# Kernel optimization log

Hardware: AMD Instinct MI355X
Metric: run time of the kernel (lower is better)

Reference implementation:

```python
import jax, jax.numpy as jnp
import numpy as np

MEM_SLOTS = 8
HEAD = 64
HEADS = 16
MEM = HEAD * HEADS          # 1024
QKV = 3 * HEAD * HEADS      # 3072
B = 4096


def _layernorm(x, g, b, eps=1e-5):
    m = jnp.mean(x, axis=-1, keepdims=True)
    v = jnp.var(x, axis=-1, keepdims=True)
    return (x - m) * jax.lax.rsqrt(v + eps) * g + b


def setup_inputs() -> dict:
    key = jax.random.key(0)
    ks = jax.random.split(key, 16)
    def gw(k, shape, scale=0.02):
        return jax.random.normal(k, shape, jnp.float32) * scale
    return {
        "input_vec": jax.random.normal(ks[0], (B, MEM), jnp.float32),
        "memory": jax.random.normal(ks[1], (B, MEM_SLOTS, MEM), jnp.float32),
        # weights stored [in, out] (transpose of torch Linear.weight; same math)
        "qkv_w": gw(ks[2], (MEM, QKV)), "qkv_b": jnp.zeros((QKV,), jnp.float32),
        "qkvn_g": jnp.ones((QKV,), jnp.float32), "qkvn_b": jnp.zeros((QKV,), jnp.float32),
        "mlp1_w": gw(ks[3], (MEM, MEM)), "mlp1_b": jnp.zeros((MEM,), jnp.float32),
        "mlp2_w": gw(ks[4], (MEM, MEM)), "mlp2_b": jnp.zeros((MEM,), jnp.float32),
        "n1_g": jnp.ones((MEM,), jnp.float32), "n1_b": jnp.zeros((MEM,), jnp.float32),
        "n2_g": jnp.ones((MEM,), jnp.float32), "n2_b": jnp.zeros((MEM,), jnp.float32),
        "inp_w": gw(ks[5], (MEM, MEM)), "inp_b": jnp.zeros((MEM,), jnp.float32),
        "ig_w": gw(ks[6], (MEM, 2 * MEM)), "ig_b": jnp.zeros((2 * MEM,), jnp.float32),
        "mg_w": gw(ks[7], (MEM, 2 * MEM)), "mg_b": jnp.zeros((2 * MEM,), jnp.float32),
        "forget_bias": jnp.asarray(1.0, jnp.float32),
        "input_bias": jnp.asarray(0.0, jnp.float32),
    }


def reference(input_vec, memory, qkv_w, qkv_b, qkvn_g, qkvn_b,
              mlp1_w, mlp1_b, mlp2_w, mlp2_b, n1_g, n1_b, n2_g, n2_b,
              inp_w, inp_b, ig_w, ig_b, mg_w, mg_b, forget_bias, input_bias):
    # project input and append as extra slot: [B, N=mem_slots+1, MEM]
    inp = (input_vec @ inp_w + inp_b)[:, None, :]
    m = jnp.concatenate([memory, inp], axis=1)
    Bsz, N, _ = m.shape

    # fused qkv + layernorm, split into heads: [B, N, H, 3, hd]
    qkv = _layernorm(m @ qkv_w + qkv_b, qkvn_g, qkvn_b).reshape(Bsz, N, HEADS, 3, HEAD)
    q, k, v = qkv[..., 0, :], qkv[..., 1, :], qkv[..., 2, :]
    scale = HEAD ** -0.5
    attn = jax.nn.softmax(jnp.einsum('bnhd,bmhd->bhnm', q * scale, k), axis=-1)
    attended = jnp.einsum('bhnm,bmhd->bnhd', attn, v).reshape(Bsz, N, MEM)

    m = _layernorm(m + attended, n1_g, n1_b)
    mlp = jax.nn.relu(m @ mlp1_w + mlp1_b) @ mlp2_w + mlp2_b
    m = _layernorm(m + mlp, n2_g, n2_b)

    next_memory = m[:, :-1, :]  # drop input slot

    # LSTM-style gating ('unit' style)
    gates = (memory @ mg_w + mg_b) + (inp @ ig_w + ig_b)  # [B, mem_slots, 2*MEM]
    i_gate, f_gate = jnp.split(gates, 2, axis=-1)
    i_gate = jax.nn.sigmoid(i_gate + input_bias)
    f_gate = jax.nn.sigmoid(f_gate + forget_bias)
    next_memory = i_gate * jnp.tanh(next_memory) + f_gate * memory

    output = next_memory.reshape(Bsz, -1)
    return output, next_memory
```

## Files before the change

### kernel.cpp

```cpp
#include <hip/hip_runtime.h>
#include <stdint.h>

typedef __attribute__((ext_vector_type(8))) short s16x8;
typedef __attribute__((ext_vector_type(4))) float f32x4;

__device__ __forceinline__ float bf2f(unsigned short u) {
  union { unsigned int i; float f; } x; x.i = ((unsigned int)u) << 16; return x.f;
}
__device__ __forceinline__ unsigned short f2bf(float f) {
  union { float f; unsigned int i; } x; x.f = f;
  return (unsigned short)((x.i + 0x7FFFu + ((x.i >> 16) & 1u)) >> 16);
}
__device__ __forceinline__ void gload16(const unsigned short* g, unsigned short* l) {
  __builtin_amdgcn_global_load_lds((const __attribute__((address_space(1))) void*)g,
                                   (__attribute__((address_space(3))) void*)l, 16, 0, 0);
}

__global__ void wtrans_kernel(const float* __restrict__ w, unsigned short* __restrict__ wt,
                              int K, int N) {
  __shared__ float tile[32][33];
  const int n0 = blockIdx.x * 32, k0 = blockIdx.y * 32;
  const int tx = threadIdx.x, ty = threadIdx.y;
  for (int r = 0; r < 32; r += 8)
    tile[ty + r][tx] = w[(size_t)(k0 + ty + r) * N + n0 + tx];
  __syncthreads();
  for (int r = 0; r < 32; r += 8)
    wt[(size_t)(n0 + ty + r) * K + k0 + tx] = f2bf(tile[tx][ty + r]);
}

__global__ void cvt_f32_bf16(const float* __restrict__ src, unsigned short* __restrict__ dst, int n4) {
  int i = blockIdx.x * blockDim.x + threadIdx.x;
  const int stride = gridDim.x * blockDim.x;
  for (; i < n4; i += stride) {
    float4 v = ((const float4*)src)[i];
    ushort4 o; o.x = f2bf(v.x); o.y = f2bf(v.y); o.z = f2bf(v.z); o.w = f2bf(v.w);
    ((ushort4*)dst)[i] = o;
  }
}

template<int AMODE, int EPI>
__global__ void __launch_bounds__(256)
gemm_bt(const unsigned short* __restrict__ A,
        const unsigned short* __restrict__ A2,
        const unsigned short* __restrict__ Bt,
        const float* __restrict__ bias,
        const unsigned short* __restrict__ igp,
        const float* __restrict__ sib,
        const float* __restrict__ sfb,
        unsigned short* __restrict__ C,
        int tilesN, int N, int K)
{
  __shared__ __align__(16) unsigned short As[128 * 32];
  __shared__ __align__(16) unsigned short Bs[128 * 32];
  const int t = threadIdx.x;
  const int w = t >> 6, l = t & 63;

  const int nwg = gridDim.x;
  const int cpx = nwg >> 3;
  const int lid = blockIdx.x;
  const int wgid = (lid & 7) * cpx + (lid >> 3);
  const int bty = wgid / tilesN;
  const int btx = wgid - bty * tilesN;
  const int brow = bty << 7, bcol = btx << 7;
  const int wr = w >> 1, wc = w & 1;

  const unsigned short* ap[2];
  const unsigned short* bp[2];
  unsigned short* al[2];
  unsigned short* bl[2];
#pragma unroll
  for (int p0 = 0; p0 < 2; ++p0) {
    const int byteoff = ((p0 * 4 + w) << 10) + (l << 4);
    const int row = byteoff >> 6;
    const int ce  = (byteoff & 63) >> 1;
    const int ar  = brow + row;
    if (AMODE == 0) {
      ap[p0] = A + (size_t)ar * K + ce;
    } else {
      const int bb = ar / 9;
      const int nn = ar - bb * 9;
      ap[p0] = (nn < 8 ? (A + ((size_t)(bb * 8 + nn)) * K) : (A2 + (size_t)bb * K)) + ce;
    }
    bp[p0] = Bt + (size_t)(bcol + row) * K + ce;
    al[p0] = As + ((p0 * 4 + w) << 9);
    bl[p0] = Bs + ((p0 * 4 + w) << 9);
  }

  f32x4 acc[4][4] = {};
  const int kiters = K >> 5;
  for (int kt = 0; kt < kiters; ++kt) {
#pragma unroll
    for (int p0 = 0; p0 < 2; ++p0) {
      gload16(ap[p0], al[p0]);
      gload16(bp[p0], bl[p0]);
      ap[p0] += 32; bp[p0] += 32;
    }
    __syncthreads();
    const int lr = l & 15, lk = (l >> 4) << 3;
    s16x8 af[4], bfr[4];
#pragma unroll
    for (int m = 0; m < 4; ++m)
      af[m] = *(const s16x8*)(As + ((wr * 64 + m * 16 + lr) << 5) + lk);
#pragma unroll
    for (int n = 0; n < 4; ++n)
      bfr[n] = *(const s16x8*)(Bs + ((wc * 64 + n * 16 + lr) << 5) + lk);
#pragma unroll
    for (int m = 0; m < 4; ++m)
#pragma unroll
      for (int n = 0; n < 4; ++n)
        acc[m][n] = __builtin_amdgcn_mfma_f32_16x16x32_bf16(af[m], bfr[n], acc[m][n], 0, 0, 0);
    __syncthreads();
  }

  float ib = 0.f, fb = 0.f;
  if constexpr (EPI == 3) { ib = sib[0]; fb = sfb[0]; }
  const int row0 = brow + wr * 64 + ((l >> 4) << 2);
  const int col0 = bcol + wc * 64 + (l & 15);
#pragma unroll
  for (int m = 0; m < 4; ++m) {
#pragma unroll
    for (int n = 0; n < 4; ++n) {
      const int col = col0 + n * 16;
      const float bv = bias[col];
#pragma unroll
      for (int j = 0; j < 4; ++j) {
        const int row = row0 + m * 16 + j;
        float x = acc[m][n][j] + bv;
        if constexpr (EPI == 1) x = fmaxf(x, 0.f);
        if constexpr (EPI == 3) {
          x += bf2f(igp[(size_t)(row >> 3) * 2048 + col]);
          x += (col < 1024) ? ib : fb;
          x = 1.f / (1.f + expf(-x));
        }
        C[(size_t)row * N + col] = f2bf(x);
      }
    }
  }
}

#define QROW 3080
__global__ void __launch_bounds__(256)
attn_fused(const unsigned short* __restrict__ qkv,
           const float* __restrict__ g3, const float* __restrict__ b3,
           const float* __restrict__ memF,
           const float* __restrict__ g1, const float* __restrict__ b1,
           unsigned short* __restrict__ m1)
{
  __shared__ __align__(16) unsigned short sQ[9 * QROW];
  __shared__ float sS[16][8][12];
  __shared__ __align__(16) unsigned short sAtt[8 * 1024];
  const int b = blockIdx.x;
  const int t = threadIdx.x;
  const int wv = t >> 6, l = t & 63;

  const unsigned short* src = qkv + (size_t)b * (9 * 3072);
  for (int i = t; i < 3456; i += 256) {
    const int r = i / 384;
    const int c = i - r * 384;
    ((uint4*)(sQ + r * QROW))[c] = ((const uint4*)src)[i];
  }
  __syncthreads();

  for (int r = wv; r < 9; r += 4) {
    float s = 0.f, s2 = 0.f;
    for (int i = l; i < 3072; i += 64) {
      const float x = bf2f(sQ[r * QROW + i]); s += x; s2 += x * x;
    }
#pragma unroll
    for (int o = 32; o; o >>= 1) { s += __shfl_xor(s, o); s2 += __shfl_xor(s2, o); }
    const float mean = s * (1.f / 3072.f);
    const float rstd = rsqrtf(s2 * (1.f / 3072.f) - mean * mean + 1e-5f);
    for (int i = l; i < 3072; i += 64) {
      const float x = bf2f(sQ[r * QROW + i]);
      sQ[r * QROW + i] = f2bf((x - mean) * rstd * g3[i] + b3[i]);
    }
  }
  __syncthreads();

  for (int idx = t; idx < 1152; idx += 256) {
    const int h = idx / 72;
    const int rem = idx - h * 72;
    const int n = rem / 9;
    const int m = rem - n * 9;
    const ushort4* q4 = (const ushort4*)(sQ + n * QROW + h * 192);
    const ushort4* k4 = (const ushort4*)(sQ + m * QROW + h * 192 + 64);
    float acc = 0.f;
#pragma unroll
    for (int d = 0; d < 16; ++d) {
      const ushort4 qa = q4[d], ka = k4[d];
      acc += bf2f(qa.x) * bf2f(ka.x) + bf2f(qa.y) * bf2f(ka.y)
           + bf2f(qa.z) * bf2f(ka.z) + bf2f(qa.w) * bf2f(ka.w);
    }
    sS[h][n][m] = acc * 0.125f;
  }
  __syncthreads();

  if (t < 128) {
    const int h = t >> 3, n = t & 7;
    float mx = -1e30f;
#pragma unroll
    for (int m = 0; m < 9; ++m) mx = fmaxf(mx, sS[h][n][m]);
    float p[9]; float sum = 0.f;
#pragma unroll
    for (int m = 0; m < 9; ++m) { p[m] = expf(sS[h][n][m] - mx); sum += p[m]; }
    const float inv = 1.f / sum;
#pragma unroll
    for (int m = 0; m < 9; ++m) sS[h][n][m] = p[m] * inv;
  }
  __syncthreads();

  for (int o4 = t; o4 < 2048; o4 += 256) {
    const int n = o4 >> 8;
    const int rem = o4 & 255;
    const int h = rem >> 4;
    const int d4 = rem & 15;
    float a0 = 0, a1 = 0, a2 = 0, a3 = 0;
#pragma unroll
    for (int m = 0; m < 9; ++m) {
      const float pm = sS[h][n][m];
      const ushort4 vv = *(const ushort4*)(sQ + m * QROW + h * 192 + 128 + d4 * 4);
      a0 += pm * bf2f(vv.x); a1 += pm * bf2f(vv.y); a2 += pm * bf2f(vv.z); a3 += pm * bf2f(vv.w);
    }
    ushort4 ov; ov.x = f2bf(a0); ov.y = f2bf(a1); ov.z = f2bf(a2); ov.w = f2bf(a3);
    ((ushort4*)sAtt)[o4] = ov;
  }
  __syncthreads();

  const float* memb = memF + (size_t)b * 8192;
  for (int n = wv; n < 8; n += 4) {
    float xs[16]; float s = 0.f, s2 = 0.f;
#pragma unroll
    for (int j = 0; j < 16; ++j) {
      const int i = j * 64 + l;
      const float x = memb[n * 1024 + i] + bf2f(sAtt[n * 1024 + i]);
      xs[j] = x; s += x; s2 += x * x;
    }
#pragma unroll
    for (int o = 32; o; o >>= 1) { s += __shfl_xor(s, o); s2 += __shfl_xor(s2, o); }
    const float mean = s * (1.f / 1024.f);
    const float rstd = rsqrtf(s2 * (1.f / 1024.f) - mean * mean + 1e-5f);
    unsigned short* dst = m1 + ((size_t)b * 8 + n) * 1024;
#pragma unroll
    for (int j = 0; j < 16; ++j) {
      const int i = j * 64 + l;
      dst[i] = f2bf((xs[j] - mean) * rstd * g1[i] + b1[i]);
    }
  }
}

__global__ void __launch_bounds__(256)
ln2_kernel(const unsigned short* __restrict__ m1, const unsigned short* __restrict__ mlp,
           const float* __restrict__ g, const float* __restrict__ bb,
           unsigned short* __restrict__ m2)
{
  const int row = blockIdx.x, t = threadIdx.x;
  const ushort4 v1 = ((const ushort4*)(m1 + (size_t)row * 1024))[t];
  const ushort4 v2 = ((const ushort4*)(mlp + (size_t)row * 1024))[t];
  const float x0 = bf2f(v1.x) + bf2f(v2.x), x1 = bf2f(v1.y) + bf2f(v2.y),
              x2 = bf2f(v1.z) + bf2f(v2.z), x3 = bf2f(v1.w) + bf2f(v2.w);
  float s = x0 + x1 + x2 + x3;
  float s2 = x0 * x0 + x1 * x1 + x2 * x2 + x3 * x3;
#pragma unroll
  for (int o = 32; o; o >>= 1) { s += __shfl_xor(s, o); s2 += __shfl_xor(s2, o); }
  __shared__ float rs[4], rq[4];
  const int wv = t >> 6, l = t & 63;
  if (l == 0) { rs[wv] = s; rq[wv] = s2; }
  __syncthreads();
  s = rs[0] + rs[1] + rs[2] + rs[3];
  s2 = rq[0] + rq[1] + rq[2] + rq[3];
  const float mean = s * (1.f / 1024.f);
  const float rstd = rsqrtf(s2 * (1.f / 1024.f) - mean * mean + 1e-5f);
  const float4 gv = ((const float4*)g)[t];
  const float4 bv = ((const float4*)bb)[t];
  ushort4 ov;
  ov.x = f2bf((x0 - mean) * rstd * gv.x + bv.x);
  ov.y = f2bf((x1 - mean) * rstd * gv.y + bv.y);
  ov.z = f2bf((x2 - mean) * rstd * gv.z + bv.z);
  ov.w = f2bf((x3 - mean) * rstd * gv.w + bv.w);
  ((ushort4*)(m2 + (size_t)row * 1024))[t] = ov;
}

__global__ void __launch_bounds__(256)
final_kernel(const unsigned short* __restrict__ sg,
             const unsigned short* __restrict__ m2,
             const float* __restrict__ memF,
             float* __restrict__ out)
{
  const int e4 = blockIdx.x * 256 + threadIdx.x;
  const int row = e4 >> 8;
  const int c4 = e4 & 255;
  const ushort4 iv = ((const ushort4*)(sg + (size_t)row * 2048))[c4];
  const ushort4 fv = ((const ushort4*)(sg + (size_t)row * 2048 + 1024))[c4];
  const ushort4 mv = ((const ushort4*)m2)[e4];
  const float4 me = ((const float4*)memF)[e4];
  float4 r;
  r.x = bf2f(iv.x) * tanhf(bf2f(mv.x)) + bf2f(fv.x) * me.x;
  r.y = bf2f(iv.y) * tanhf(bf2f(mv.y)) + bf2f(fv.y) * me.y;
  r.z = bf2f(iv.z) * tanhf(bf2f(mv.z)) + bf2f(fv.z) * me.z;
  r.w = bf2f(iv.w) * tanhf(bf2f(mv.w)) + bf2f(fv.w) * me.w;
  ((float4*)out)[e4] = r;
  ((float4*)out)[8388608 + e4] = r;
}

extern "C" void kernel_launch(void* const* d_in, const int* in_sizes, int n_in,
                              void* d_out, int out_size, void* d_ws, size_t ws_size,
                              hipStream_t stream) {
  (void)in_sizes; (void)n_in; (void)out_size; (void)ws_size;
  const float* input_vec = (const float*)d_in[0];
  const float* memory    = (const float*)d_in[1];
  const float* qkv_w  = (const float*)d_in[2];
  const float* qkv_b  = (const float*)d_in[3];
  const float* qkvn_g = (const float*)d_in[4];
  const float* qkvn_b = (const float*)d_in[5];
  const float* mlp1_w = (const float*)d_in[6];
  const float* mlp1_b = (const float*)d_in[7];
  const float* mlp2_w = (const float*)d_in[8];
  const float* mlp2_b = (const float*)d_in[9];
  const float* n1_g = (const float*)d_in[10];
  const float* n1_b = (const float*)d_in[11];
  const float* n2_g = (const float*)d_in[12];
  const float* n2_b = (const float*)d_in[13];
  const float* inp_w = (const float*)d_in[14];
  const float* inp_b = (const float*)d_in[15];
  const float* ig_w  = (const float*)d_in[16];
  const float* ig_b  = (const float*)d_in[17];
  const float* mg_w  = (const float*)d_in[18];
  const float* mg_b  = (const float*)d_in[19];
  const float* forget_bias = (const float*)d_in[20];
  const float* input_bias  = (const float*)d_in[21];

  char* p = (char*)d_ws;
  auto carve = [&](size_t bytes) -> void* {
    void* r = (void*)p; p += (bytes + 255) & ~(size_t)255; return r;
  };
  unsigned short* mem_bf  = (unsigned short*)carve(67108864);
  unsigned short* iv_bf   = (unsigned short*)carve(8388608);
  unsigned short* inp_bf  = (unsigned short*)carve(8388608);
  unsigned short* inp_wT  = (unsigned short*)carve(2097152);
  unsigned short* qkv_wT  = (unsigned short*)carve(6291456);
  unsigned short* mlp1_wT = (unsigned short*)carve(2097152);
  unsigned short* mlp2_wT = (unsigned short*)carve(2097152);
  unsigned short* ig_wT   = (unsigned short*)carve(4194304);
  unsigned short* mg_wT   = (unsigned short*)carve(4194304);
  char* big               = (char*)carve(226492416);
  unsigned short* qkv_pre = (unsigned short*)big;
  unsigned short* gates   = (unsigned short*)big;
  unsigned short* mlp_buf = (unsigned short*)(big + 134217728);
  unsigned short* m1      = (unsigned short*)carve(67108864);
  unsigned short* h_buf   = (unsigned short*)carve(67108864);
  unsigned short* m2      = h_buf;
  unsigned short* ig_part = (unsigned short*)carve(16777216);

  const dim3 tb(32, 8);
  wtrans_kernel<<<dim3(32, 32), tb, 0, stream>>>(inp_w,  inp_wT,  1024, 1024);
  wtrans_kernel<<<dim3(96, 32), tb, 0, stream>>>(qkv_w,  qkv_wT,  1024, 3072);
  wtrans_kernel<<<dim3(32, 32), tb, 0, stream>>>(mlp1_w, mlp1_wT, 1024, 1024);
  wtrans_kernel<<<dim3(32, 32), tb, 0, stream>>>(mlp2_w, mlp2_wT, 1024, 1024);
  wtrans_kernel<<<dim3(64, 32), tb, 0, stream>>>(ig_w,   ig_wT,   1024, 2048);
  wtrans_kernel<<<dim3(64, 32), tb, 0, stream>>>(mg_w,   mg_wT,   1024, 2048);
  cvt_f32_bf16<<<2048, 256, 0, stream>>>(input_vec, iv_bf, 1048576);
  cvt_f32_bf16<<<2048, 256, 0, stream>>>(memory, mem_bf, 8388608);

  gemm_bt<0, 0><<<256, 256, 0, stream>>>(iv_bf, nullptr, inp_wT, inp_b,
      nullptr, nullptr, nullptr, inp_bf, 8, 1024, 1024);
  gemm_bt<1, 0><<<6912, 256, 0, stream>>>(mem_bf, inp_bf, qkv_wT, qkv_b,
      nullptr, nullptr, nullptr, qkv_pre, 24, 3072, 1024);
  attn_fused<<<4096, 256, 0, stream>>>(qkv_pre, qkvn_g, qkvn_b, memory, n1_g, n1_b, m1);
  gemm_bt<0, 1><<<2048, 256, 0, stream>>>(m1, nullptr, mlp1_wT, mlp1_b,
      nullptr, nullptr, nullptr, h_buf, 8, 1024, 1024);
  gemm_bt<0, 0><<<2048, 256, 0, stream>>>(h_buf, nullptr, mlp2_wT, mlp2_b,
      nullptr, nullptr, nullptr, mlp_buf, 8, 1024, 1024);
  ln2_kernel<<<32768, 256, 0, stream>>>(m1, mlp_buf, n2_g, n2_b, m2);
  gemm_bt<0, 0><<<512, 256, 0, stream>>>(inp_bf, nullptr, ig_wT, ig_b,
      nullptr, nullptr, nullptr, ig_part, 16, 2048, 1024);
  gemm_bt<0, 3><<<4096, 256, 0, stream>>>(mem_bf, nullptr, mg_wT, mg_b,
      ig_part, input_bias, forget_bias, gates, 16, 2048, 1024);
  final_kernel<<<32768, 256, 0, stream>>>(gates, m2, memory, (float*)d_out);
}
```

Baseline: 1.647 ms.

## Add 256x128-tile triple-buffered MFMA GEMM for the large GEMMs

```diff
diff --git a/kernel.cpp b/kernel.cpp
--- a/kernel.cpp
+++ b/kernel.cpp
@@ -35,6 +35,175 @@
     float4 v = ((const float4*)src)[i];
     ushort4 o; o.x = f2bf(v.x); o.y = f2bf(v.y); o.z = f2bf(v.z); o.w = f2bf(v.w);
     ((ushort4*)dst)[i] = o;
+  }
+}
+
+template<int AMODE, int EPI>
+__global__ void __launch_bounds__(512, 2)
+gemm3(const unsigned short* __restrict__ A,
+      const unsigned short* __restrict__ A2,
+      const unsigned short* __restrict__ Bt,
+      const float* __restrict__ bias,
+      const unsigned short* __restrict__ igp,
+      const float* __restrict__ sib,
+      const float* __restrict__ sfb,
+      unsigned short* __restrict__ C,
+      int tilesN, int N, int K)
+{
+  __shared__ __align__(16) unsigned short lds[3 * 24576];
+  const int tid = threadIdx.x;
+  const int w = tid >> 6, l = tid & 63;
+  const int lr = l & 15, lg = l >> 4;
+
+  const int nwg = gridDim.x;
+  const int cpx = nwg >> 3;
+  const int lid = blockIdx.x;
+  const int wgid = (lid & 7) * cpx + (lid >> 3);
+  const int bty = wgid / tilesN;
+  const int btx = wgid - bty * tilesN;
+  const int brow = bty << 8;
+  const int bcol = btx << 7;
+  const int wr = w >> 2, wc = w & 3;
+
+  const unsigned short* gsrc[6];
+  int ldst[6];
+  {
+    const int sub = tid >> 3;
+    const int kbs = ((tid & 7) << 4) ^ ((sub & 7) << 4);
+#pragma unroll
+    for (int c = 0; c < 6; ++c) {
+      if (c < 4) {
+        const int gr = brow + c * 64 + sub;
+        const unsigned short* rp;
+        if (AMODE == 0) {
+          rp = A + (size_t)gr * K;
+        } else {
+          const int bb = gr / 9;
+          const int nn = gr - bb * 9;
+          rp = (nn < 8) ? (A + ((size_t)(bb * 8 + nn)) * K) : (A2 + (size_t)bb * K);
+        }
+        gsrc[c] = rp + (kbs >> 1);
+        ldst[c] = c * 4096 + (w << 9);
+      } else {
+        const int gc = bcol + (c - 4) * 64 + sub;
+        gsrc[c] = Bt + (size_t)gc * K + (kbs >> 1);
+        ldst[c] = 16384 + (c - 4) * 4096 + (w << 9);
+      }
+    }
+  }
+
+  const int swr = (lr & 7) << 4;
+  int aoff[8][2], boff[2][2];
+#pragma unroll
+  for (int m = 0; m < 8; ++m)
+#pragma unroll
+    for (int kk = 0; kk < 2; ++kk) {
+      const int row = wr * 128 + m * 16 + lr;
+      aoff[m][kk] = row * 64 + ((((kk << 6) | (lg << 4)) ^ swr) >> 1);
+    }
+#pragma unroll
+  for (int n = 0; n < 2; ++n)
+#pragma unroll
+    for (int kk = 0; kk < 2; ++kk) {
+      const int col = wc * 32 + n * 16 + lr;
+      boff[n][kk] = 16384 + col * 64 + ((((kk << 6) | (lg << 4)) ^ swr) >> 1);
+    }
+
+  f32x4 acc[8][2] = {};
+  const int NT = K >> 6;
+
+#pragma unroll
+  for (int c = 0; c < 6; ++c) gload16(gsrc[c], lds + ldst[c]);
+#pragma unroll
+  for (int c = 0; c < 6; ++c) gload16(gsrc[c] + 64, lds + 24576 + ldst[c]);
+  asm volatile("s_waitcnt vmcnt(6)" ::: "memory");
+  __builtin_amdgcn_s_barrier();
+
+  int s = 0;
+  for (int t = 0; t < NT; ++t) {
+    const int sBase  = s * 24576;
+    const int s2Base = ((s >= 1) ? (s - 1) : (s + 2)) * 24576;
+    const bool pf = (t + 2 < NT);
+    const int ktn = (t + 2) << 6;
+
+    if (pf) {
+      gload16(gsrc[0] + ktn, lds + s2Base + ldst[0]);
+      gload16(gsrc[1] + ktn, lds + s2Base + ldst[1]);
+      gload16(gsrc[2] + ktn, lds + s2Base + ldst[2]);
+    }
+    s16x8 bfr[2][2], af[4][2];
+#pragma unroll
+    for (int n = 0; n < 2; ++n)
+#pragma unroll
+      for (int kk = 0; kk < 2; ++kk)
+        bfr[n][kk] = *(const s16x8*)(lds + sBase + boff[n][kk]);
+#pragma unroll
+    for (int m = 0; m < 4; ++m)
+#pragma unroll
+      for (int kk = 0; kk < 2; ++kk)
+        af[m][kk] = *(const s16x8*)(lds + sBase + aoff[m][kk]);
+    asm volatile("s_barrier" ::: "memory");
+    __builtin_amdgcn_s_setprio(1);
+#pragma unroll
+    for (int kk = 0; kk < 2; ++kk)
+#pragma unroll
+      for (int m = 0; m < 4; ++m)
+#pragma unroll
+        for (int n = 0; n < 2; ++n)
+          acc[m][n] = __builtin_amdgcn_mfma_f32_16x16x32_bf16(af[m][kk], bfr[n][kk], acc[m][n], 0, 0, 0);
+    __builtin_amdgcn_s_setprio(0);
+    asm volatile("s_barrier" ::: "memory");
+
+    if (pf) {
+      gload16(gsrc[3] + ktn, lds + s2Base + ldst[3]);
+      gload16(gsrc[4] + ktn, lds + s2Base + ldst[4]);
+      gload16(gsrc[5] + ktn, lds + s2Base + ldst[5]);
+    }
+    s16x8 ag[4][2];
+#pragma unroll
+    for (int m = 0; m < 4; ++m)
+#pragma unroll
+      for (int kk = 0; kk < 2; ++kk)
+        ag[m][kk] = *(const s16x8*)(lds + sBase + aoff[m + 4][kk]);
+    asm volatile("s_barrier" ::: "memory");
+    __builtin_amdgcn_s_setprio(1);
+#pragma unroll
+    for (int kk = 0; kk < 2; ++kk)
+#pragma unroll
+      for (int m = 0; m < 4; ++m)
+#pragma unroll
+        for (int n = 0; n < 2; ++n)
+          acc[m + 4][n] = __builtin_amdgcn_mfma_f32_16x16x32_bf16(ag[m][kk], bfr[n][kk], acc[m + 4][n], 0, 0, 0);
+    __builtin_amdgcn_s_setprio(0);
+    if (pf)                 asm volatile("s_waitcnt vmcnt(6)\ns_barrier" ::: "memory");
+    else if (t + 1 < NT)    asm volatile("s_waitcnt vmcnt(0)\ns_barrier" ::: "memory");
+    else                    asm volatile("s_barrier" ::: "memory");
+    s = (s == 2) ? 0 : s + 1;
+  }
+
+  float ib = 0.f, fb = 0.f;
+  if constexpr (EPI == 3) { ib = sib[0]; fb = sfb[0]; }
+  const int row0 = brow + wr * 128 + (lg << 2);
+  const int col0 = bcol + wc * 32 + lr;
+#pragma unroll
+  for (int m = 0; m < 8; ++m) {
+#pragma unroll
+    for (int n = 0; n < 2; ++n) {
+      const int col = col0 + n * 16;
+      const float bv = bias[col];
+#pragma unroll
+      for (int j = 0; j < 4; ++j) {
+        const int row = row0 + m * 16 + j;
+        float x = acc[m][n][j] + bv;
+        if constexpr (EPI == 1) x = fmaxf(x, 0.f);
+        if constexpr (EPI == 3) {
+          x += bf2f(igp[(size_t)(row >> 3) * 2048 + col]);
+          x += (col < 1024) ? ib : fb;
+          x = 1.f / (1.f + expf(-x));
+        }
+        C[(size_t)row * N + col] = f2bf(x);
+      }
+    }
   }
 }
 
@@ -363,17 +532,17 @@
 
   gemm_bt<0, 0><<<256, 256, 0, stream>>>(iv_bf, nullptr, inp_wT, inp_b,
       nullptr, nullptr, nullptr, inp_bf, 8, 1024, 1024);
-  gemm_bt<1, 0><<<6912, 256, 0, stream>>>(mem_bf, inp_bf, qkv_wT, qkv_b,
+  gemm3<1, 0><<<3456, 512, 0, stream>>>(mem_bf, inp_bf, qkv_wT, qkv_b,
       nullptr, nullptr, nullptr, qkv_pre, 24, 3072, 1024);
   attn_fused<<<4096, 256, 0, stream>>>(qkv_pre, qkvn_g, qkvn_b, memory, n1_g, n1_b, m1);
-  gemm_bt<0, 1><<<2048, 256, 0, stream>>>(m1, nullptr, mlp1_wT, mlp1_b,
+  gemm3<0, 1><<<1024, 512, 0, stream>>>(m1, nullptr, mlp1_wT, mlp1_b,
       nullptr, nullptr, nullptr, h_buf, 8, 1024, 1024);
-  gemm_bt<0, 0><<<2048, 256, 0, stream>>>(h_buf, nullptr, mlp2_wT, mlp2_b,
+  gemm3<0, 0><<<1024, 512, 0, stream>>>(h_buf, nullptr, mlp2_wT, mlp2_b,
       nullptr, nullptr, nullptr, mlp_buf, 8, 1024, 1024);
   ln2_kernel<<<32768, 256, 0, stream>>>(m1, mlp_buf, n2_g, n2_b, m2);
   gemm_bt<0, 0><<<512, 256, 0, stream>>>(inp_bf, nullptr, ig_wT, ig_b,
       nullptr, nullptr, nullptr, ig_part, 16, 2048, 1024);
-  gemm_bt<0, 3><<<4096, 256, 0, stream>>>(mem_bf, nullptr, mg_wT, mg_b,
+  gemm3<0, 3><<<2048, 512, 0, stream>>>(mem_bf, nullptr, mg_wT, mg_b,
       ig_part, input_bias, forget_bias, gates, 16, 2048, 1024);
   final_kernel<<<32768, 256, 0, stream>>>(gates, m2, memory, (float*)d_out);
 }
```

After: 1.501 ms. -8.9%, faster.

## Add 256x256 double-buffered MFMA GEMM and fuse LN2 with gating output

Applied to the files above, without the earlier changes.

```diff
diff --git a/kernel.cpp b/kernel.cpp
--- a/kernel.cpp
+++ b/kernel.cpp
@@ -35,6 +35,182 @@
     float4 v = ((const float4*)src)[i];
     ushort4 o; o.x = f2bf(v.x); o.y = f2bf(v.y); o.z = f2bf(v.z); o.w = f2bf(v.w);
     ((ushort4*)dst)[i] = o;
+  }
+}
+
+template<int AMODE, int EPI>
+__global__ void __launch_bounds__(512, 2)
+gemm4(const unsigned short* __restrict__ A,
+      const unsigned short* __restrict__ A2,
+      const unsigned short* __restrict__ Bt,
+      const float* __restrict__ bias,
+      const unsigned short* __restrict__ igp,
+      const float* __restrict__ sib,
+      const float* __restrict__ sfb,
+      unsigned short* __restrict__ C,
+      int tilesN, int N, int K)
+{
+  __shared__ __align__(16) unsigned short lds[2 * 32768];
+  const int tid = threadIdx.x;
+  const int w = tid >> 6, l = tid & 63;
+  const int lr = l & 15, lg = l >> 4;
+
+  const int nwg = gridDim.x;
+  const int cpx = nwg >> 3;
+  const int lid = blockIdx.x;
+  const int wgid = (lid & 7) * cpx + (lid >> 3);
+  const int bty = wgid / tilesN;
+  const int btx = wgid - bty * tilesN;
+  const int brow = bty << 8;
+  const int bcol = btx << 8;
+  const int wr = w >> 2, wc = w & 3;
+
+  const int sub = tid >> 3;
+  const int kbs = ((tid & 7) << 4) ^ ((sub & 7) << 4);
+  const size_t kstep64 = (size_t)64 * K;
+
+  const unsigned short* aP[2];
+  const unsigned short* aQ[2];
+  const unsigned short* bP[2];
+#pragma unroll
+  for (int h = 0; h < 2; ++h) {
+    if (AMODE == 0) {
+      aP[h] = A + (size_t)(brow + h * 128 + sub) * K + (kbs >> 1);
+      aQ[h] = nullptr;
+    } else {
+#pragma unroll
+      for (int i = 0; i < 2; ++i) {
+        const int gr = brow + h * 128 + i * 64 + sub;
+        const int bb = gr / 9;
+        const int nn = gr - bb * 9;
+        const unsigned short* rp =
+            (nn < 8) ? (A + ((size_t)(bb * 8 + nn)) * K) : (A2 + (size_t)bb * K);
+        if (i == 0) aP[h] = rp + (kbs >> 1); else aQ[h] = rp + (kbs >> 1);
+      }
+    }
+    bP[h] = Bt + (size_t)(bcol + h * 128 + sub) * K + (kbs >> 1);
+  }
+  const int ldb = w << 9;
+
+  auto stage_a = [&](int h, int slotB, int kofs) {
+    const unsigned short* s1 = (AMODE == 0) ? (aP[h] + kstep64 + kofs) : (aQ[h] + kofs);
+    gload16(aP[h] + kofs, lds + slotB + h * 8192 + ldb);
+    gload16(s1,           lds + slotB + h * 8192 + 4096 + ldb);
+  };
+  auto stage_b = [&](int h, int slotB, int kofs) {
+    gload16(bP[h] + kofs,           lds + slotB + 16384 + h * 8192 + ldb);
+    gload16(bP[h] + kstep64 + kofs, lds + slotB + 16384 + h * 8192 + 4096 + ldb);
+  };
+
+  const int swr = (lr & 7) << 4;
+  const int kpart0 = (((lg << 4)) ^ swr) >> 1;
+  const int kpart1 = ((64 | (lg << 4)) ^ swr) >> 1;
+
+  f32x4 acc[8][4] = {};
+  const int NT = K >> 6;
+
+  stage_a(0, 0, 0); stage_a(1, 0, 0); stage_b(0, 0, 0); stage_b(1, 0, 0);
+  stage_a(0, 32768, 64); stage_a(1, 32768, 64);
+  asm volatile("s_waitcnt vmcnt(4)" ::: "memory");
+  __builtin_amdgcn_s_barrier();
+
+#define MFMA_Q(AF, BF, RB, CB)                                                  \
+  _Pragma("unroll") for (int kk = 0; kk < 2; ++kk)                              \
+  _Pragma("unroll") for (int m = 0; m < 4; ++m)                                 \
+  _Pragma("unroll") for (int n = 0; n < 2; ++n)                                 \
+    acc[(RB) + m][(CB) + n] = __builtin_amdgcn_mfma_f32_16x16x32_bf16(          \
+        AF[m][kk], BF[n][kk], acc[(RB) + m][(CB) + n], 0, 0, 0);
+
+  int cur = 0;
+  for (int t = 0; t < NT; ++t) {
+    const int curB = cur << 15;
+    const int nxtB = curB ^ 32768;
+    const unsigned short* As = lds + curB;
+    const unsigned short* Bs = As + 16384;
+    const int k1 = (t + 1) << 6, k2 = (t + 2) << 6;
+    const bool p1 = (t + 1 < NT), p2 = (t + 2 < NT);
+
+    if (p1) stage_b(0, nxtB, k1);
+    s16x8 a0[4][2], b0[2][2];
+#pragma unroll
+    for (int m = 0; m < 4; ++m) {
+      const int ro = (wr * 128 + m * 16 + lr) * 64;
+      a0[m][0] = *(const s16x8*)(As + ro + kpart0);
+      a0[m][1] = *(const s16x8*)(As + ro + kpart1);
+    }
+#pragma unroll
+    for (int n = 0; n < 2; ++n) {
+      const int co = (wc * 64 + n * 16 + lr) * 64;
+      b0[n][0] = *(const s16x8*)(Bs + co + kpart0);
+      b0[n][1] = *(const s16x8*)(Bs + co + kpart1);
+    }
+    asm volatile("s_barrier" ::: "memory");
+    __builtin_amdgcn_s_setprio(1);
+    MFMA_Q(a0, b0, 0, 0)
+    __builtin_amdgcn_s_setprio(0);
+    asm volatile("s_barrier" ::: "memory");
+
+    if (p1) stage_b(1, nxtB, k1);
+    s16x8 a1[4][2], b1[2][2];
+#pragma unroll
+    for (int m = 0; m < 4; ++m) {
+      const int ro = (wr * 128 + 64 + m * 16 + lr) * 64;
+      a1[m][0] = *(const s16x8*)(As + ro + kpart0);
+      a1[m][1] = *(const s16x8*)(As + ro + kpart1);
+    }
+#pragma unroll
+    for (int n = 0; n < 2; ++n) {
+      const int co = (wc * 64 + 32 + n * 16 + lr) * 64;
+      b1[n][0] = *(const s16x8*)(Bs + co + kpart0);
+      b1[n][1] = *(const s16x8*)(Bs + co + kpart1);
+    }
+    asm volatile("s_barrier" ::: "memory");
+    __builtin_amdgcn_s_setprio(1);
+    MFMA_Q(a0, b1, 0, 2)
+    __builtin_amdgcn_s_setprio(0);
+    asm volatile("s_barrier" ::: "memory");
+
+    if (p2) stage_a(0, curB, k2);
+    __builtin_amdgcn_s_setprio(1);
+    MFMA_Q(a1, b0, 4, 0)
+    __builtin_amdgcn_s_setprio(0);
+
+    if (p2) stage_a(1, curB, k2);
+    __builtin_amdgcn_s_setprio(1);
+    MFMA_Q(a1, b1, 4, 2)
+    __builtin_amdgcn_s_setprio(0);
+    if (p2)      asm volatile("s_waitcnt vmcnt(4)\ns_barrier" ::: "memory");
+    else if (p1) asm volatile("s_waitcnt vmcnt(0)\ns_barrier" ::: "memory");
+    else         asm volatile("s_barrier" ::: "memory");
+    cur ^= 1;
+  }
+#undef MFMA_Q
+
+  float ib = 0.f, fb = 0.f;
+  if constexpr (EPI == 3) { ib = sib[0]; fb = sfb[0]; }
+  const int row0 = brow + wr * 128 + (lg << 2);
+  const int col0 = bcol + wc * 64 + lr;
+#pragma unroll
+  for (int i = 0; i < 8; ++i) {
+    const int qm = i >> 2, m = i & 3;
+#pragma unroll
+    for (int jq = 0; jq < 4; ++jq) {
+      const int qn = jq >> 1, n = jq & 1;
+      const int col = col0 + qn * 32 + n * 16;
+      const float bv = bias[col];
+#pragma unroll
+      for (int j = 0; j < 4; ++j) {
+        const int row = row0 + qm * 64 + m * 16 + j;
+        float x = acc[i][jq][j] + bv;
+        if constexpr (EPI == 1) x = fmaxf(x, 0.f);
+        if constexpr (EPI == 3) {
+          x += bf2f(igp[(size_t)(row >> 3) * 2048 + col]);
+          x += (col < 1024) ? ib : fb;
+          x = 1.f / (1.f + expf(-x));
+        }
+        C[(size_t)row * N + col] = f2bf(x);
+      }
+    }
   }
 }
 
@@ -249,9 +425,11 @@
 }
 
 __global__ void __launch_bounds__(256)
-ln2_kernel(const unsigned short* __restrict__ m1, const unsigned short* __restrict__ mlp,
-           const float* __restrict__ g, const float* __restrict__ bb,
-           unsigned short* __restrict__ m2)
+ln2_final(const unsigned short* __restrict__ m1, const unsigned short* __restrict__ mlp,
+          const float* __restrict__ g, const float* __restrict__ bb,
+          const unsigned short* __restrict__ sg,
+          const float* __restrict__ memF,
+          float* __restrict__ out)
 {
   const int row = blockIdx.x, t = threadIdx.x;
   const ushort4 v1 = ((const ushort4*)(m1 + (size_t)row * 1024))[t];
@@ -272,34 +450,20 @@
   const float rstd = rsqrtf(s2 * (1.f / 1024.f) - mean * mean + 1e-5f);
   const float4 gv = ((const float4*)g)[t];
   const float4 bv = ((const float4*)bb)[t];
-  ushort4 ov;
-  ov.x = f2bf((x0 - mean) * rstd * gv.x + bv.x);
-  ov.y = f2bf((x1 - mean) * rstd * gv.y + bv.y);
-  ov.z = f2bf((x2 - mean) * rstd * gv.z + bv.z);
-  ov.w = f2bf((x3 - mean) * rstd * gv.w + bv.w);
-  ((ushort4*)(m2 + (size_t)row * 1024))[t] = ov;
-}
-
-__global__ void __launch_bounds__(256)
-final_kernel(const unsigned short* __restrict__ sg,
-             const unsigned short* __restrict__ m2,
-             const float* __restrict__ memF,
-             float* __restrict__ out)
-{
-  const int e4 = blockIdx.x * 256 + threadIdx.x;
-  const int row = e4 >> 8;
-  const int c4 = e4 & 255;
-  const ushort4 iv = ((const ushort4*)(sg + (size_t)row * 2048))[c4];
-  const ushort4 fv = ((const ushort4*)(sg + (size_t)row * 2048 + 1024))[c4];
-  const ushort4 mv = ((const ushort4*)m2)[e4];
-  const float4 me = ((const float4*)memF)[e4];
+  const float m20 = (x0 - mean) * rstd * gv.x + bv.x;
+  const float m21 = (x1 - mean) * rstd * gv.y + bv.y;
+  const float m22 = (x2 - mean) * rstd * gv.z + bv.z;
+  const float m23 = (x3 - mean) * rstd * gv.w + bv.w;
+  const ushort4 iv = ((const ushort4*)(sg + (size_t)row * 2048))[t];
+  const ushort4 fv = ((const ushort4*)(sg + (size_t)row * 2048 + 1024))[t];
+  const float4 me = ((const float4*)(memF + (size_t)row * 1024))[t];
   float4 r;
-  r.x = bf2f(iv.x) * tanhf(bf2f(mv.x)) + bf2f(fv.x) * me.x;
-  r.y = bf2f(iv.y) * tanhf(bf2f(mv.y)) + bf2f(fv.y) * me.y;
-  r.z = bf2f(iv.z) * tanhf(bf2f(mv.z)) + bf2f(fv.z) * me.z;
-  r.w = bf2f(iv.w) * tanhf(bf2f(mv.w)) + bf2f(fv.w) * me.w;
-  ((float4*)out)[e4] = r;
-  ((float4*)out)[8388608 + e4] = r;
+  r.x = bf2f(iv.x) * tanhf(m20) + bf2f(fv.x) * me.x;
+  r.y = bf2f(iv.y) * tanhf(m21) + bf2f(fv.y) * me.y;
+  r.z = bf2f(iv.z) * tanhf(m22) + bf2f(fv.z) * me.z;
+  r.w = bf2f(iv.w) * tanhf(m23) + bf2f(fv.w) * me.w;
+  ((float4*)out)[(size_t)row * 256 + t] = r;
+  ((float4*)out)[8388608 + (size_t)row * 256 + t] = r;
 }
 
 extern "C" void kernel_launch(void* const* d_in, const int* in_sizes, int n_in,
@@ -348,7 +512,6 @@
   unsigned short* mlp_buf = (unsigned short*)(big + 134217728);
   unsigned short* m1      = (unsigned short*)carve(67108864);
   unsigned short* h_buf   = (unsigned short*)carve(67108864);
-  unsigned short* m2      = h_buf;
   unsigned short* ig_part = (unsigned short*)carve(16777216);
 
   const dim3 tb(32, 8);
@@ -363,17 +526,16 @@
 
   gemm_bt<0, 0><<<256, 256, 0, stream>>>(iv_bf, nullptr, inp_wT, inp_b,
       nullptr, nullptr, nullptr, inp_bf, 8, 1024, 1024);
-  gemm_bt<1, 0><<<6912, 256, 0, stream>>>(mem_bf, inp_bf, qkv_wT, qkv_b,
-      nullptr, nullptr, nullptr, qkv_pre, 24, 3072, 1024);
+  gemm4<1, 0><<<1728, 512, 0, stream>>>(mem_bf, inp_bf, qkv_wT, qkv_b,
+      nullptr, nullptr, nullptr, qkv_pre, 12, 3072, 1024);
   attn_fused<<<4096, 256, 0, stream>>>(qkv_pre, qkvn_g, qkvn_b, memory, n1_g, n1_b, m1);
-  gemm_bt<0, 1><<<2048, 256, 0, stream>>>(m1, nullptr, mlp1_wT, mlp1_b,
-      nullptr, nullptr, nullptr, h_buf, 8, 1024, 1024);
-  gemm_bt<0, 0><<<2048, 256, 0, stream>>>(h_buf, nullptr, mlp2_wT, mlp2_b,
-      nullptr, nullptr, nullptr, mlp_buf, 8, 1024, 1024);
-  ln2_kernel<<<32768, 256, 0, stream>>>(m1, mlp_buf, n2_g, n2_b, m2);
+  gemm4<0, 1><<<512, 512, 0, stream>>>(m1, nullptr, mlp1_wT, mlp1_b,
+      nullptr, nullptr, nullptr, h_buf, 4, 1024, 1024);
+  gemm4<0, 0><<<512, 512, 0, stream>>>(h_buf, nullptr, mlp2_wT, mlp2_b,
+      nullptr, nullptr, nullptr, mlp_buf, 4, 1024, 1024);
   gemm_bt<0, 0><<<512, 256, 0, stream>>>(inp_bf, nullptr, ig_wT, ig_b,
       nullptr, nullptr, nullptr, ig_part, 16, 2048, 1024);
-  gemm_bt<0, 3><<<4096, 256, 0, stream>>>(mem_bf, nullptr, mg_wT, mg_b,
-      ig_part, input_bias, forget_bias, gates, 16, 2048, 1024);
-  final_kernel<<<32768, 256, 0, stream>>>(gates, m2, memory, (float*)d_out);
-}
+  gemm4<0, 3><<<1024, 512, 0, stream>>>(mem_bf, nullptr, mg_wT, mg_b,
+      ig_part, input_bias, forget_bias, gates, 8, 2048, 1024);
+  ln2_final<<<32768, 256, 0, stream>>>(m1, mlp_buf, n2_g, n2_b, gates, memory, (float*)d_out);
+}
```

After: 1.438 ms. 12.7% less time.
